# Optimization experiments

Hardware: AMD Instinct MI355X
Metric: run time of the kernel (lower is better)

Reference implementation:

```python
import jax, jax.numpy as jnp
import numpy as np

DIM = 1024
HEADS = 16
HEAD_DIM = DIM // HEADS
MLP_HIDDEN = 4 * DIM
OUT_DIM = 1000
V_DIM = 1024
EPS = 1e-5
SCALE = DIM ** -0.5  # note: module scales by hidden_dim**-0.5, not head_dim**-0.5


def layer_norm(x, g, b):
    mu = jnp.mean(x, axis=-1, keepdims=True)
    var = jnp.mean(jnp.square(x - mu), axis=-1, keepdims=True)
    return (x - mu) * jax.lax.rsqrt(var + EPS) * g + b


def setup_inputs() -> dict:
    key = jax.random.key(0)
    ks = jax.random.split(key, 12)
    B, N = 4, 2048
    s = lambda fan_in: 1.0 / np.sqrt(fan_in)
    return {
        "x": jax.random.normal(ks[0], (B, N, DIM), jnp.float32),
        "value": jax.random.normal(ks[1], (B, N, V_DIM), jnp.float32),
        "wq": jax.random.normal(ks[2], (DIM, DIM), jnp.float32) * s(DIM),
        "wk": jax.random.normal(ks[3], (DIM, DIM), jnp.float32) * s(DIM),
        "wv": jax.random.normal(ks[4], (V_DIM, DIM), jnp.float32) * s(V_DIM),
        "w_ap": jax.random.normal(ks[5], (DIM, DIM), jnp.float32) * s(DIM),
        "b_ap": jnp.zeros((DIM,), jnp.float32),
        "g1": jnp.ones((DIM,), jnp.float32),
        "be1": jnp.zeros((DIM,), jnp.float32),
        "g2": jnp.ones((DIM,), jnp.float32),
        "be2": jnp.zeros((DIM,), jnp.float32),
        "w1": jax.random.normal(ks[6], (DIM, MLP_HIDDEN), jnp.float32) * s(DIM),
        "b1": jnp.zeros((MLP_HIDDEN,), jnp.float32),
        "w2": jax.random.normal(ks[7], (MLP_HIDDEN, DIM), jnp.float32) * s(MLP_HIDDEN),
        "b2": jnp.zeros((DIM,), jnp.float32),
        "w_out": jax.random.normal(ks[8], (DIM, OUT_DIM), jnp.float32) * s(DIM),
        "b_out": jnp.zeros((OUT_DIM,), jnp.float32),
    }


def reference(x, value, wq, wk, wv, w_ap, b_ap, g1, be1, g2, be2, w1, b1, w2, b2, w_out, b_out):
    B, N, C = x.shape
    xn = layer_norm(x, g1, be1)                      # [B,N,C]
    q = (xn @ wq).reshape(B, N, HEADS, HEAD_DIM)     # query and key both from norm1(x)
    k = (xn @ wk).reshape(B, N, HEADS, HEAD_DIM)
    v = (value @ wv).reshape(B, N, HEADS, HEAD_DIM)
    attn = jnp.einsum("bqhd,bkhd->bhqk", q, k) * SCALE
    attn = jax.nn.softmax(attn, axis=-1)
    o = jnp.einsum("bhqk,bkhd->bqhd", attn, v).reshape(B, N, C)
    x = x + (o @ w_ap + b_ap)                        # residual (dropouts are identity)
    h = jax.nn.gelu(layer_norm(x, g2, be2) @ w1 + b1, approximate=False)
    x = x + (h @ w2 + b2)
    return jax.nn.softmax(x @ w_out + b_out, axis=2)
```

## Files before the change

kernel.cpp:

```cpp
#include <hip/hip_runtime.h>
#include <math.h>

typedef unsigned short u16;
typedef unsigned int u32;
typedef __attribute__((ext_vector_type(4))) float f32x4;
typedef __attribute__((ext_vector_type(4))) int i32x4;
typedef __attribute__((ext_vector_type(8))) short short8;
typedef __attribute__((ext_vector_type(4))) unsigned short u16x4;
typedef __attribute__((ext_vector_type(4))) __fp16 f16x4;
typedef __attribute__((ext_vector_type(2))) __fp16 f16x2;

#define DEV __device__ __forceinline__

DEV u16 f2bf(float f) {
  unsigned u = __float_as_uint(f);
  u += 0x7FFFu + ((u >> 16) & 1u);
  return (u16)(u >> 16);
}

DEV float fexp2(float x) {
  float r;
  asm("v_exp_f32 %0, %1" : "=v"(r) : "v"(x));
  return r;
}

DEV void gload_lds16(const void* g, void* l) {
  __builtin_amdgcn_global_load_lds((const __attribute__((address_space(1))) void*)g,
                                   (__attribute__((address_space(3))) void*)l, 16, 0, 0);
}

enum { EPI_QK = 0, EPI_VT = 1, EPI_RESID_F32 = 2, EPI_GELU = 3, EPI_RESID_BF16 = 4, EPI_LOGITS = 5 };

__global__ void transpose_w(const float* __restrict__ in, u16* __restrict__ out,
                            int K, int Nsrc, int Nout) {
  __shared__ float tile[32][33];
  int k0 = blockIdx.x * 32, n0 = blockIdx.y * 32;
  int tx = threadIdx.x, ty = threadIdx.y;
#pragma unroll
  for (int i = 0; i < 4; ++i) {
    int k = k0 + ty + i * 8, n = n0 + tx;
    tile[ty + i * 8][tx] = (n < Nsrc) ? in[(size_t)k * Nsrc + n] : 0.0f;
  }
  __syncthreads();
#pragma unroll
  for (int i = 0; i < 4; ++i) {
    int n = n0 + ty + i * 8, k = k0 + tx;
    out[(size_t)n * K + k] = f2bf(tile[tx][ty + i * 8]);
  }
}

__global__ void convert_bf16(const float* __restrict__ in, u16* __restrict__ out, int n4) {
  int i = blockIdx.x * blockDim.x + threadIdx.x;
  int stride = gridDim.x * blockDim.x;
  for (int j = i; j < n4; j += stride) {
    f32x4 v = reinterpret_cast<const f32x4*>(in)[j];
    u16x4 o;
    o[0] = f2bf(v[0]); o[1] = f2bf(v[1]); o[2] = f2bf(v[2]); o[3] = f2bf(v[3]);
    reinterpret_cast<u16x4*>(out)[j] = o;
  }
}

DEV float blockReduceSum(float v) {
  __shared__ float red[4];
#pragma unroll
  for (int m = 32; m >= 1; m >>= 1) v += __shfl_xor(v, m);
  __syncthreads();
  if ((threadIdx.x & 63) == 0) red[threadIdx.x >> 6] = v;
  __syncthreads();
  return red[0] + red[1] + red[2] + red[3];
}

DEV float blockReduceMax(float v) {
  __shared__ float redm[4];
#pragma unroll
  for (int m = 32; m >= 1; m >>= 1) v = fmaxf(v, __shfl_xor(v, m));
  __syncthreads();
  if ((threadIdx.x & 63) == 0) redm[threadIdx.x >> 6] = v;
  __syncthreads();
  return fmaxf(fmaxf(redm[0], redm[1]), fmaxf(redm[2], redm[3]));
}

__global__ __launch_bounds__(256)
void layernorm_k(const float* __restrict__ x, const float* __restrict__ g,
                 const float* __restrict__ b, u16* __restrict__ out) {
  int row = blockIdx.x, t = threadIdx.x;
  const float* xr = x + (size_t)row * 1024;
  f32x4 v = *reinterpret_cast<const f32x4*>(xr + t * 4);
  float mu = blockReduceSum(v[0] + v[1] + v[2] + v[3]) * (1.0f / 1024.0f);
  f32x4 d;
  d[0] = v[0] - mu; d[1] = v[1] - mu; d[2] = v[2] - mu; d[3] = v[3] - mu;
  float var = blockReduceSum(d[0]*d[0] + d[1]*d[1] + d[2]*d[2] + d[3]*d[3]) * (1.0f / 1024.0f);
  float rstd = rsqrtf(var + 1e-5f);
  u16x4 o;
#pragma unroll
  for (int i = 0; i < 4; ++i) o[i] = f2bf(d[i] * rstd * g[t * 4 + i] + b[t * 4 + i]);
  *reinterpret_cast<u16x4*>(out + (size_t)row * 1024 + t * 4) = o;
}

__global__ __launch_bounds__(256)
void softmax_rows(float* __restrict__ io) {
  int row = blockIdx.x, t = threadIdx.x;
  float* p = io + (size_t)row * 1000;
  float v[4];
  float mx = -INFINITY;
#pragma unroll
  for (int i = 0; i < 4; ++i) {
    int c = t + i * 256;
    v[i] = (c < 1000) ? p[c] : -INFINITY;
    mx = fmaxf(mx, v[i]);
  }
  mx = blockReduceMax(mx);
  float s = 0.f;
#pragma unroll
  for (int i = 0; i < 4; ++i) {
    int c = t + i * 256;
    v[i] = (c < 1000) ? __expf(v[i] - mx) : 0.f;
    s += v[i];
  }
  s = blockReduceSum(s);
  float inv = 1.0f / s;
#pragma unroll
  for (int i = 0; i < 4; ++i) {
    int c = t + i * 256;
    if (c < 1000) p[c] = v[i] * inv;
  }
}

template<int EPI>
__global__ __launch_bounds__(256)
void gemm_bt(const u16* __restrict__ A, const u16* __restrict__ Bt,
             void* __restrict__ outp, const float* __restrict__ aux0,
             const float* __restrict__ aux1, int M, int N, int K, float scale) {
  __shared__ u16 As[2][128 * 64];
  __shared__ u16 Bs[2][128 * 64];
  const int t = threadIdx.x;
  const int lane = t & 63;
  const int w = t >> 6;
  const int wm = w >> 1, wn = w & 1;
  const int bm = blockIdx.y * 128, bn = blockIdx.x * 128;
  const int l15 = lane & 15, lg = lane >> 4;

  f32x4 acc[4][4] = {};

  const int r0 = t >> 3;
  const int sg = ((t & 7) ^ ((t >> 3) & 7)) * 8;

  auto STAGE = [&](int buf, int kt) {
#pragma unroll
    for (int p = 0; p < 4; ++p) {
      int r = p * 32 + r0;
      gload_lds16(A  + (size_t)(bm + r) * K + kt + sg, &As[buf][p * 2048 + t * 8]);
      gload_lds16(Bt + (size_t)(bn + r) * K + kt + sg, &Bs[buf][p * 2048 + t * 8]);
    }
  };

  auto COMPUTE = [&](int buf) {
#pragma unroll
    for (int ks = 0; ks < 2; ++ks) {
      short8 af[4], bfr[4];
#pragma unroll
      for (int i = 0; i < 4; ++i) {
        int rA = wm * 64 + i * 16 + l15;
        int sa = (lg + ks * 4) ^ (rA & 7);
        af[i] = *reinterpret_cast<const short8*>(&As[buf][rA * 64 + sa * 8]);
        int rB = wn * 64 + i * 16 + l15;
        int sb = (lg + ks * 4) ^ (rB & 7);
        bfr[i] = *reinterpret_cast<const short8*>(&Bs[buf][rB * 64 + sb * 8]);
      }
#pragma unroll
      for (int i = 0; i < 4; ++i)
#pragma unroll
        for (int j = 0; j < 4; ++j)
          acc[i][j] = __builtin_amdgcn_mfma_f32_16x16x32_bf16(af[i], bfr[j], acc[i][j], 0, 0, 0);
    }
  };

  const int nk = K >> 6;
  STAGE(0, 0);
  __syncthreads();
#pragma unroll 1
  for (int i = 0; i + 1 < nk; ++i) {
    STAGE((i + 1) & 1, (i + 1) << 6);
    COMPUTE(i & 1);
    __syncthreads();
  }
  COMPUTE((nk - 1) & 1);

#pragma unroll
  for (int i = 0; i < 4; ++i)
#pragma unroll
    for (int j = 0; j < 4; ++j)
#pragma unroll
      for (int r = 0; r < 4; ++r) {
        int row = bm + wm * 64 + i * 16 + lg * 4 + r;
        int col = bn + wn * 64 + j * 16 + l15;
        float v = acc[i][j][r];
        if constexpr (EPI == EPI_QK) {
          float sc = (col < 1024) ? 0.03125f : 1.0f;
          ((u16*)outp)[(size_t)row * 2048 + col] = f2bf(v * sc);
        } else if constexpr (EPI == EPI_VT) {
          size_t idx = ((size_t)((row >> 11) * 16 + (col >> 6)) * 64 + (col & 63)) * 2048 + (row & 2047);
          __fp16 hv = (__fp16)v;
          ((u16*)outp)[idx] = *reinterpret_cast<u16*>(&hv);
        } else if constexpr (EPI == EPI_RESID_F32) {
          ((float*)outp)[(size_t)row * N + col] = v + aux0[col] + aux1[(size_t)row * N + col];
        } else if constexpr (EPI == EPI_GELU) {
          float tt = v + aux0[col];
          float u = tt * (0.7978845608f + 0.035677408f * tt * tt);
          float e = fexp2(u * 2.8853900818f);
          float gl = tt * (1.0f - 1.0f / (1.0f + e));
          ((u16*)outp)[(size_t)row * N + col] = f2bf(gl);
        } else if constexpr (EPI == EPI_RESID_BF16) {
          float tt = v + aux0[col] + aux1[(size_t)row * N + col];
          ((u16*)outp)[(size_t)row * N + col] = f2bf(tt);
        } else {
          if (col < 1000) ((float*)outp)[(size_t)row * 1000 + col] = v + aux0[col];
        }
      }
  (void)scale; (void)aux0; (void)aux1; (void)M;
}

__global__ __launch_bounds__(512)
void attn_flash(const u16* __restrict__ QKb, const u16* __restrict__ Vt,
                u16* __restrict__ Ob) {
  __shared__ u16 Ks[2][128 * 64];
  __shared__ u16 Vs[2][64 * 128];
  const int t = threadIdx.x;
  const int lane = t & 63, w = t >> 6;
  const int l15 = lane & 15, lg = lane >> 4;
  const int bh = blockIdx.x;
  const int b = bh >> 4, h = bh & 15;
  const int qrow0 = b * 2048 + blockIdx.y * 128 + w * 16;

  short8 qf[2];
#pragma unroll
  for (int ks = 0; ks < 2; ++ks)
    qf[ks] = *reinterpret_cast<const short8*>(QKb + (size_t)(qrow0 + l15) * 2048 + h * 64 + ks * 32 + lg * 8);

  f32x4 oacc[4] = {};
  float lpart = 0.f;

  const int sgK = ((t & 7) ^ ((t >> 3) & 7)) * 8;
  const int sgV = ((t & 15) ^ ((t >> 4) & 7)) * 8;
  const int tk8 = t * 8;

  auto STAGE = [&](int buf, int tt) {
    int kt = tt * 128;
#pragma unroll
    for (int p = 0; p < 2; ++p) {
      int rK = p * 64 + (t >> 3);
      gload_lds16(QKb + (size_t)(b * 2048 + kt + rK) * 2048 + 1024 + h * 64 + sgK, &Ks[buf][p * 4096 + tk8]);
      int rV = p * 32 + (t >> 4);
      gload_lds16(Vt + ((size_t)bh * 64 + rV) * 2048 + kt + sgV, &Vs[buf][p * 4096 + tk8]);
    }
  };

  auto COMPUTE = [&](int buf) {
    f32x4 s[8];
#pragma unroll
    for (int cb = 0; cb < 8; ++cb) {
      s[cb] = f32x4{0.f, 0.f, 0.f, 0.f};
      int rK = cb * 16 + l15;
#pragma unroll
      for (int ks = 0; ks < 2; ++ks) {
        int sk = (lg + ks * 4) ^ (rK & 7);
        short8 kf = *reinterpret_cast<const short8*>(&Ks[buf][rK * 64 + sk * 8]);
        s[cb] = __builtin_amdgcn_mfma_f32_16x16x32_bf16(kf, qf[ks], s[cb], 0, 0, 0);
      }
    }

    const float L2E = 1.44269504088896f;
    const char* vbase = (const char*)&Vs[buf][0];
#pragma unroll
    for (int cb = 0; cb < 8; ++cb) {
      float e0 = fexp2(s[cb][0] * L2E), e1 = fexp2(s[cb][1] * L2E);
      float e2 = fexp2(s[cb][2] * L2E), e3 = fexp2(s[cb][3] * L2E);
      lpart += (e0 + e1) + (e2 + e3);
      f16x2 plo = __builtin_amdgcn_cvt_pkrtz(e0, e1);
      f16x2 phi = __builtin_amdgcn_cvt_pkrtz(e2, e3);
      f16x4 pf;
      pf[0] = plo[0]; pf[1] = plo[1]; pf[2] = phi[0]; pf[3] = phi[1];
#pragma unroll
      for (int db = 0; db < 4; ++db) {
        int d = db * 16 + l15;
        int boff = d * 256 + ((((2 * cb + (lg >> 1)) ^ (d & 7)) << 4) | ((lg & 1) << 3));
        f16x4 vf = *reinterpret_cast<const f16x4*>(vbase + boff);
        oacc[db] = __builtin_amdgcn_mfma_f32_16x16x16f16(pf, vf, oacc[db], 0, 0, 0);
      }
    }
  };

  STAGE(0, 0);
  __syncthreads();
#pragma unroll 1
  for (int i = 0; i < 8; ++i) {
    STAGE(1, 2 * i + 1);
    COMPUTE(0);
    __syncthreads();
    if (i < 7) STAGE(0, 2 * i + 2);
    COMPUTE(1);
    __syncthreads();
  }

  lpart += __shfl_xor(lpart, 16);
  lpart += __shfl_xor(lpart, 32);
  float inv = 1.0f / lpart;
  float invr[4];
#pragma unroll
  for (int r = 0; r < 4; ++r) invr[r] = __shfl(inv, lg * 4 + r);

#pragma unroll
  for (int db = 0; db < 4; ++db)
#pragma unroll
    for (int r = 0; r < 4; ++r) {
      int row = qrow0 + lg * 4 + r;
      int col = h * 64 + db * 16 + l15;
      Ob[(size_t)row * 1024 + col] = f2bf(oacc[db][r] * invr[r]);
    }
}

extern "C" void kernel_launch(void* const* d_in, const int* in_sizes, int n_in,
                              void* d_out, int out_size, void* d_ws, size_t ws_size,
                              hipStream_t stream) {
  (void)in_sizes; (void)n_in; (void)out_size; (void)ws_size;
  const float* x     = (const float*)d_in[0];
  const float* value = (const float*)d_in[1];
  const float* wq    = (const float*)d_in[2];
  const float* wk    = (const float*)d_in[3];
  const float* wv    = (const float*)d_in[4];
  const float* w_ap  = (const float*)d_in[5];
  const float* b_ap  = (const float*)d_in[6];
  const float* g1    = (const float*)d_in[7];
  const float* be1   = (const float*)d_in[8];
  const float* g2    = (const float*)d_in[9];
  const float* be2   = (const float*)d_in[10];
  const float* w1    = (const float*)d_in[11];
  const float* b1    = (const float*)d_in[12];
  const float* w2    = (const float*)d_in[13];
  const float* b2    = (const float*)d_in[14];
  const float* w_out = (const float*)d_in[15];
  const float* b_out = (const float*)d_in[16];

  char* ws = (char*)d_ws;
  u16* wqT   = (u16*)(ws + 0x0000000);
  u16* wkT   = (u16*)(ws + 0x0200000);
  u16* wvT   = (u16*)(ws + 0x0400000);
  u16* wapT  = (u16*)(ws + 0x0600000);
  u16* woutT = (u16*)(ws + 0x0800000);
  u16* w1T   = (u16*)(ws + 0x0A00000);
  u16* w2T   = (u16*)(ws + 0x1200000);
  u16* xn    = (u16*)(ws + 0x1A00000);
  u16* valb  = (u16*)(ws + 0x2A00000);
  u16* qkb   = (u16*)(ws + 0x3A00000);
  u16* vT    = (u16*)(ws + 0x5A00000);
  u16* ob    = (u16*)(ws + 0x6A00000);
  float* x1  = (float*)(ws + 0x7A00000);
  u16* hb    = valb;
  u16* xn2   = xn;
  u16* x2b   = ob;

  dim3 tb(32, 8);
  transpose_w<<<dim3(32, 32),  tb, 0, stream>>>(wq,    wqT,   1024, 1024, 1024);
  transpose_w<<<dim3(32, 32),  tb, 0, stream>>>(wk,    wkT,   1024, 1024, 1024);
  transpose_w<<<dim3(32, 32),  tb, 0, stream>>>(wv,    wvT,   1024, 1024, 1024);
  transpose_w<<<dim3(32, 32),  tb, 0, stream>>>(w_ap,  wapT,  1024, 1024, 1024);
  transpose_w<<<dim3(32, 32),  tb, 0, stream>>>(w_out, woutT, 1024, 1000, 1024);
  transpose_w<<<dim3(32, 128), tb, 0, stream>>>(w1,    w1T,   1024, 4096, 4096);
  transpose_w<<<dim3(128, 32), tb, 0, stream>>>(w2,    w2T,   4096, 1024, 1024);

  convert_bf16<<<2048, 256, 0, stream>>>(value, valb, 2097152);
  layernorm_k<<<8192, 256, 0, stream>>>(x, g1, be1, xn);

  gemm_bt<EPI_QK><<<dim3(16, 64), 256, 0, stream>>>(xn,   wqT, qkb, nullptr, nullptr, 8192, 2048, 1024, 1.0f);
  gemm_bt<EPI_VT><<<dim3(8, 64),  256, 0, stream>>>(valb, wvT, vT,  nullptr, nullptr, 8192, 1024, 1024, 1.0f);

  attn_flash<<<dim3(64, 16), 512, 0, stream>>>(qkb, vT, ob);

  gemm_bt<EPI_RESID_F32><<<dim3(8, 64),  256, 0, stream>>>(ob,  wapT, x1, b_ap, x, 8192, 1024, 1024, 1.0f);
  layernorm_k<<<8192, 256, 0, stream>>>(x1, g2, be2, xn2);
  gemm_bt<EPI_GELU>     <<<dim3(32, 64), 256, 0, stream>>>(xn2, w1T, hb, b1, nullptr, 8192, 4096, 1024, 1.0f);
  gemm_bt<EPI_RESID_BF16><<<dim3(8, 64), 256, 0, stream>>>(hb,  w2T, x2b, b2, x1, 8192, 1024, 4096, 1.0f);
  gemm_bt<EPI_LOGITS>   <<<dim3(8, 64),  256, 0, stream>>>(x2b, woutT, (float*)d_out, b_out, nullptr, 8192, 1024, 1024, 1.0f);
  softmax_rows<<<8192, 256, 0, stream>>>((float*)d_out);
}
```

Measured before the change: 480.4 us.

## Replace GEMM with 4-stage pipelined 256-row tiles and 512 threads

```diff
diff --git a/kernel.cpp b/kernel.cpp
--- a/kernel.cpp
+++ b/kernel.cpp
@@ -27,6 +27,20 @@
 DEV void gload_lds16(const void* g, void* l) {
   __builtin_amdgcn_global_load_lds((const __attribute__((address_space(1))) void*)g,
                                    (__attribute__((address_space(3))) void*)l, 16, 0, 0);
+}
+
+template<int N> DEV void waitv() {
+  if constexpr (N == 8)      asm volatile("s_waitcnt vmcnt(8)" ::: "memory");
+  else if constexpr (N == 6) asm volatile("s_waitcnt vmcnt(6)" ::: "memory");
+  else if constexpr (N == 4) asm volatile("s_waitcnt vmcnt(4)" ::: "memory");
+  else if constexpr (N == 3) asm volatile("s_waitcnt vmcnt(3)" ::: "memory");
+  else                       asm volatile("s_waitcnt vmcnt(0)" ::: "memory");
+}
+
+DEV void block_fence() {
+  __builtin_amdgcn_s_barrier();
+  __builtin_amdgcn_sched_barrier(0);
+  asm volatile("" ::: "memory");
 }
 
 enum { EPI_QK = 0, EPI_VT = 1, EPI_RESID_F32 = 2, EPI_GELU = 3, EPI_RESID_BF16 = 4, EPI_LOGITS = 5 };
@@ -126,74 +140,95 @@
   }
 }
 
-template<int EPI>
-__global__ __launch_bounds__(256)
-void gemm_bt(const u16* __restrict__ A, const u16* __restrict__ Bt,
-             void* __restrict__ outp, const float* __restrict__ aux0,
-             const float* __restrict__ aux1, int M, int N, int K, float scale) {
-  __shared__ u16 As[2][128 * 64];
-  __shared__ u16 Bs[2][128 * 64];
+template<int EPI, int BN>
+__global__ __launch_bounds__(512, 1)
+void gemm_pipe(const u16* __restrict__ A, const u16* __restrict__ Bt,
+               void* __restrict__ outp, const float* __restrict__ aux0,
+               const float* __restrict__ aux1, int M, int N, int K, float scale) {
+  constexpr int ASZ = 256 * 32;
+  constexpr int BSZ = BN * 32;
+  constexpr int NJ  = BN / 64;
+  constexpr int LPT = (BN == 256) ? 4 : 3;
+  __shared__ u16 lds[4][ASZ + BSZ];
+
   const int t = threadIdx.x;
   const int lane = t & 63;
   const int w = t >> 6;
-  const int wm = w >> 1, wn = w & 1;
-  const int bm = blockIdx.y * 128, bn = blockIdx.x * 128;
+  const int wm = w >> 2, wn = w & 3;
+  const int bm = blockIdx.y * 256, bn = blockIdx.x * BN;
   const int l15 = lane & 15, lg = lane >> 4;
-
-  f32x4 acc[4][4] = {};
-
-  const int r0 = t >> 3;
-  const int sg = ((t & 7) ^ ((t >> 3) & 7)) * 8;
+  const int nk = K >> 5;
+
+  f32x4 acc[8][NJ] = {};
 
   auto STAGE = [&](int buf, int kt) {
-#pragma unroll
-    for (int p = 0; p < 4; ++p) {
-      int r = p * 32 + r0;
-      gload_lds16(A  + (size_t)(bm + r) * K + kt + sg, &As[buf][p * 2048 + t * 8]);
-      gload_lds16(Bt + (size_t)(bn + r) * K + kt + sg, &Bs[buf][p * 2048 + t * 8]);
+    const int k0 = kt * 32;
+#pragma unroll
+    for (int p = 0; p < 2; ++p) {
+      int c = p * 512 + t;
+      int r = c >> 2, s0 = c & 3;
+      int ss = s0 ^ ((r >> 1) & 3);
+      gload_lds16(A + (size_t)(bm + r) * K + k0 + ss * 8, &lds[buf][c * 8]);
+    }
+    if constexpr (BN == 256) {
+#pragma unroll
+      for (int p = 0; p < 2; ++p) {
+        int c = p * 512 + t;
+        int r = c >> 2, s0 = c & 3;
+        int ss = s0 ^ ((r >> 1) & 3);
+        gload_lds16(Bt + (size_t)(bn + r) * K + k0 + ss * 8, &lds[buf][ASZ + c * 8]);
+      }
+    } else {
+      int r = t >> 2, s0 = t & 3;
+      int ss = s0 ^ ((r >> 1) & 3);
+      gload_lds16(Bt + (size_t)(bn + r) * K + k0 + ss * 8, &lds[buf][ASZ + t * 8]);
     }
   };
 
-  auto COMPUTE = [&](int buf) {
-#pragma unroll
-    for (int ks = 0; ks < 2; ++ks) {
-      short8 af[4], bfr[4];
-#pragma unroll
-      for (int i = 0; i < 4; ++i) {
-        int rA = wm * 64 + i * 16 + l15;
-        int sa = (lg + ks * 4) ^ (rA & 7);
-        af[i] = *reinterpret_cast<const short8*>(&As[buf][rA * 64 + sa * 8]);
-        int rB = wn * 64 + i * 16 + l15;
-        int sb = (lg + ks * 4) ^ (rB & 7);
-        bfr[i] = *reinterpret_cast<const short8*>(&Bs[buf][rB * 64 + sb * 8]);
-      }
-#pragma unroll
-      for (int i = 0; i < 4; ++i)
-#pragma unroll
-        for (int j = 0; j < 4; ++j)
-          acc[i][j] = __builtin_amdgcn_mfma_f32_16x16x32_bf16(af[i], bfr[j], acc[i][j], 0, 0, 0);
-    }
-  };
-
-  const int nk = K >> 6;
   STAGE(0, 0);
-  __syncthreads();
+  STAGE(1, 1);
+  STAGE(2, 2);
+  waitv<2 * LPT>();
+  block_fence();
+
 #pragma unroll 1
-  for (int i = 0; i + 1 < nk; ++i) {
-    STAGE((i + 1) & 1, (i + 1) << 6);
-    COMPUTE(i & 1);
-    __syncthreads();
-  }
-  COMPUTE((nk - 1) & 1);
-
-#pragma unroll
-  for (int i = 0; i < 4; ++i)
-#pragma unroll
-    for (int j = 0; j < 4; ++j)
+  for (int tt = 0; tt < nk; ++tt) {
+    const int buf = tt & 3;
+    short8 af[8], bf[NJ];
+#pragma unroll
+    for (int i = 0; i < 8; ++i) {
+      int rA = wm * 128 + i * 16 + l15;
+      af[i] = *reinterpret_cast<const short8*>(&lds[buf][rA * 32 + (lg ^ ((rA >> 1) & 3)) * 8]);
+    }
+#pragma unroll
+    for (int j = 0; j < NJ; ++j) {
+      int rB = wn * (BN / 4) + j * 16 + l15;
+      bf[j] = *reinterpret_cast<const short8*>(&lds[buf][ASZ + rB * 32 + (lg ^ ((rB >> 1) & 3)) * 8]);
+    }
+    if (tt + 3 < nk) STAGE((tt + 3) & 3, tt + 3);
+
+    __builtin_amdgcn_s_setprio(1);
+#pragma unroll
+    for (int i = 0; i < 8; ++i)
+#pragma unroll
+      for (int j = 0; j < NJ; ++j)
+        acc[i][j] = __builtin_amdgcn_mfma_f32_16x16x32_bf16(af[i], bf[j], acc[i][j], 0, 0, 0);
+    __builtin_amdgcn_s_setprio(0);
+
+    if (tt + 3 < nk)      waitv<2 * LPT>();
+    else if (tt + 2 < nk) waitv<LPT>();
+    else if (tt + 1 < nk) waitv<0>();
+    block_fence();
+  }
+
+#pragma unroll
+  for (int i = 0; i < 8; ++i)
+#pragma unroll
+    for (int j = 0; j < NJ; ++j)
 #pragma unroll
       for (int r = 0; r < 4; ++r) {
-        int row = bm + wm * 64 + i * 16 + lg * 4 + r;
-        int col = bn + wn * 64 + j * 16 + l15;
+        int row = bm + wm * 128 + i * 16 + lg * 4 + r;
+        int col = bn + wn * (BN / 4) + j * 16 + l15;
         float v = acc[i][j][r];
         if constexpr (EPI == EPI_QK) {
           float sc = (col < 1024) ? 0.03125f : 1.0f;
@@ -205,14 +240,14 @@
         } else if constexpr (EPI == EPI_RESID_F32) {
           ((float*)outp)[(size_t)row * N + col] = v + aux0[col] + aux1[(size_t)row * N + col];
         } else if constexpr (EPI == EPI_GELU) {
-          float tt = v + aux0[col];
-          float u = tt * (0.7978845608f + 0.035677408f * tt * tt);
+          float tt2 = v + aux0[col];
+          float u = tt2 * (0.7978845608f + 0.035677408f * tt2 * tt2);
           float e = fexp2(u * 2.8853900818f);
-          float gl = tt * (1.0f - 1.0f / (1.0f + e));
+          float gl = tt2 * (1.0f - 1.0f / (1.0f + e));
           ((u16*)outp)[(size_t)row * N + col] = f2bf(gl);
         } else if constexpr (EPI == EPI_RESID_BF16) {
-          float tt = v + aux0[col] + aux1[(size_t)row * N + col];
-          ((u16*)outp)[(size_t)row * N + col] = f2bf(tt);
+          float tt2 = v + aux0[col] + aux1[(size_t)row * N + col];
+          ((u16*)outp)[(size_t)row * N + col] = f2bf(tt2);
         } else {
           if (col < 1000) ((float*)outp)[(size_t)row * 1000 + col] = v + aux0[col];
         }
@@ -371,15 +406,15 @@
   convert_bf16<<<2048, 256, 0, stream>>>(value, valb, 2097152);
   layernorm_k<<<8192, 256, 0, stream>>>(x, g1, be1, xn);
 
-  gemm_bt<EPI_QK><<<dim3(16, 64), 256, 0, stream>>>(xn,   wqT, qkb, nullptr, nullptr, 8192, 2048, 1024, 1.0f);
-  gemm_bt<EPI_VT><<<dim3(8, 64),  256, 0, stream>>>(valb, wvT, vT,  nullptr, nullptr, 8192, 1024, 1024, 1.0f);
+  gemm_pipe<EPI_QK, 256><<<dim3(8, 32),  512, 0, stream>>>(xn,   wqT, qkb, nullptr, nullptr, 8192, 2048, 1024, 1.0f);
+  gemm_pipe<EPI_VT, 128><<<dim3(8, 32),  512, 0, stream>>>(valb, wvT, vT,  nullptr, nullptr, 8192, 1024, 1024, 1.0f);
 
   attn_flash<<<dim3(64, 16), 512, 0, stream>>>(qkb, vT, ob);
 
-  gemm_bt<EPI_RESID_F32><<<dim3(8, 64),  256, 0, stream>>>(ob,  wapT, x1, b_ap, x, 8192, 1024, 1024, 1.0f);
+  gemm_pipe<EPI_RESID_F32, 128><<<dim3(8, 32),  512, 0, stream>>>(ob,  wapT, x1, b_ap, x, 8192, 1024, 1024, 1.0f);
   layernorm_k<<<8192, 256, 0, stream>>>(x1, g2, be2, xn2);
-  gemm_bt<EPI_GELU>     <<<dim3(32, 64), 256, 0, stream>>>(xn2, w1T, hb, b1, nullptr, 8192, 4096, 1024, 1.0f);
-  gemm_bt<EPI_RESID_BF16><<<dim3(8, 64), 256, 0, stream>>>(hb,  w2T, x2b, b2, x1, 8192, 1024, 4096, 1.0f);
-  gemm_bt<EPI_LOGITS>   <<<dim3(8, 64),  256, 0, stream>>>(x2b, woutT, (float*)d_out, b_out, nullptr, 8192, 1024, 1024, 1.0f);
+  gemm_pipe<EPI_GELU, 256>     <<<dim3(16, 32), 512, 0, stream>>>(xn2, w1T, hb, b1, nullptr, 8192, 4096, 1024, 1.0f);
+  gemm_pipe<EPI_RESID_BF16, 128><<<dim3(8, 32), 512, 0, stream>>>(hb,  w2T, x2b, b2, x1, 8192, 1024, 4096, 1.0f);
+  gemm_pipe<EPI_LOGITS, 128>   <<<dim3(8, 32),  512, 0, stream>>>(x2b, woutT, (float*)d_out, b_out, nullptr, 8192, 1024, 1024, 1.0f);
   softmax_rows<<<8192, 256, 0, stream>>>((float*)d_out);
 }
```

After: 468.1 us. 2.6% less time.
